# Performance work log

Hardware: AMD Instinct MI355X
Metric: run time of the kernel (lower is better)

## Reference

```python
import jax, jax.numpy as jnp
import numpy as np


def setup_inputs() -> dict:
    key = jax.random.key(0)
    k1, k2 = jax.random.split(key)
    shape = (16, 3, 512, 512)
    y_true = jax.random.uniform(k1, shape, dtype=jnp.float32)
    y_pred = jax.random.uniform(k2, shape, dtype=jnp.float32)
    return {"y_true": y_true, "y_pred": y_pred}


def reference(y_true, y_pred):
    B, C, W, H = y_true.shape
    percent = 0.4
    index = int(W * H * percent - 1)  # quantile index into ascending sort
    # gray1 = mean over the 3 channels of y_pred  -> [B, W, H]
    gray = (y_pred[:, 0] + y_pred[:, 1] + y_pred[:, 2]) / 3.0
    # torch.topk(-gray, n)[0][:, index] == -(ascending-sorted gray)[index]
    thr = jnp.sort(gray.reshape(B, W * H), axis=1)[:, index]  # [B]
    mask = (gray <= thr[:, None, None]).astype(y_pred.dtype)  # [B, W, H]
    mask = mask[:, None, :, :]  # broadcast over 3 channels
    # mask*|y_pred - y_true| == |mask*y_pred - mask*y_true| since mask in {0,1}
    d = jnp.abs(y_pred - y_true)
    w = mask * 0.8 + (1.0 - mask) * 0.2
    return jnp.mean(w * d)
```

## Files before the change

### kernel.cpp

```cpp
#include <hip/hip_runtime.h>
#include <stdint.h>

#define NB 16
#define NPIX 262144
#define K_RANK 104856u
#define NB1 4096
#define PAD(i) ((i) + ((i) >> 4))

__global__ void k_gray_hist(const float* __restrict__ yp, float* __restrict__ gray,
                            unsigned* __restrict__ hist1,
                            unsigned* __restrict__ zr, int zcount) {
    __shared__ unsigned h[NB1];
    const int tid = threadIdx.x;
    const int gtid = blockIdx.x * 256 + tid;
    if (gtid < zcount) zr[gtid] = 0;
    for (int i = tid; i < NB1; i += 256) h[i] = 0;
    __syncthreads();

    const int blk   = blockIdx.x;
    const int b     = blk >> 8;
    const int chunk = blk & 255;
    const long base = (long)b * 3 * NPIX;
    const int  o    = (chunk * 256 + tid) * 4;

    const float4 c0 = *(const float4*)(yp + base + o);
    const float4 c1 = *(const float4*)(yp + base + NPIX + o);
    const float4 c2 = *(const float4*)(yp + base + 2 * NPIX + o);

    float g0 = (c0.x + c1.x + c2.x) / 3.0f;
    float g1 = (c0.y + c1.y + c2.y) / 3.0f;
    float g2 = (c0.z + c1.z + c2.z) / 3.0f;
    float g3 = (c0.w + c1.w + c2.w) / 3.0f;

    if (gray) {
        *(float4*)(gray + (long)b * NPIX + o) = make_float4(g0, g1, g2, g3);
    }
    atomicAdd(&h[__float_as_uint(g0) >> 20], 1u);
    atomicAdd(&h[__float_as_uint(g1) >> 20], 1u);
    atomicAdd(&h[__float_as_uint(g2) >> 20], 1u);
    atomicAdd(&h[__float_as_uint(g3) >> 20], 1u);
    __syncthreads();

    unsigned* gh = hist1 + b * NB1;
    for (int i = tid; i < NB1; i += 256) {
        unsigned v = h[i];
        if (v) atomicAdd(&gh[i], v);
    }
}

__global__ void k_refine(const float* __restrict__ gray, const float* __restrict__ yp,
                         const unsigned* __restrict__ hist_scan,
                         const unsigned* __restrict__ rank_in,
                         const unsigned* __restrict__ prefix_in,
                         int width, int sel_shift, int dig_shift, unsigned dmask,
                         unsigned* __restrict__ hist_out, int nbins_out,
                         unsigned* __restrict__ rank_out, unsigned* __restrict__ prefix_out) {
    __shared__ unsigned sh[NB1 + (NB1 >> 4)];
    __shared__ unsigned wave_sums[4];
    __shared__ unsigned bc_prefix;
    const int tid   = threadIdx.x;
    const int blk   = blockIdx.x;
    const int b     = blk >> 8;
    const int chunk = blk & 255;

    const unsigned* hb = hist_scan + b * NB1;
    for (int i = tid; i < NB1; i += 256) sh[PAD(i)] = hb[i];
    __syncthreads();

    unsigned sum = 0;
    #pragma unroll
    for (int j = 0; j < 16; ++j) sum += sh[tid * 17 + j];
    unsigned inc = sum;
    for (int off = 1; off < 64; off <<= 1) {
        unsigned v = __shfl_up(inc, off);
        if ((tid & 63) >= off) inc += v;
    }
    if ((tid & 63) == 63) wave_sums[tid >> 6] = inc;
    __syncthreads();
    unsigned woff = 0;
    for (int w = 0; w < (tid >> 6); ++w) woff += wave_sums[w];
    const unsigned excl = woff + inc - sum;

    const unsigned r = rank_in ? rank_in[b] : K_RANK;
    const unsigned p = prefix_in ? prefix_in[b] : 0u;
    if (r >= excl && r < excl + sum) {
        unsigned cum = excl;
        unsigned d   = (unsigned)(tid * 16);
        #pragma unroll
        for (int j = 0; j < 16; ++j) {
            unsigned c = sh[tid * 17 + j];
            if (cum + c > r) { d = (unsigned)(tid * 16 + j); break; }
            cum += c;
        }
        bc_prefix = (p << width) | d;
        if (chunk == 0) { rank_out[b] = r - cum; prefix_out[b] = bc_prefix; }
    }
    __syncthreads();
    const unsigned pre = bc_prefix;

    for (int i = tid; i < nbins_out; i += 256) sh[i] = 0;
    __syncthreads();

    const int o = (chunk * 256 + tid) * 4;
    float g0, g1, g2, g3;
    if (gray) {
        float4 gv = *(const float4*)(gray + (long)b * NPIX + o);
        g0 = gv.x; g1 = gv.y; g2 = gv.z; g3 = gv.w;
    } else {
        const long base = (long)b * 3 * NPIX;
        float4 c0 = *(const float4*)(yp + base + o);
        float4 c1 = *(const float4*)(yp + base + NPIX + o);
        float4 c2 = *(const float4*)(yp + base + 2 * NPIX + o);
        g0 = (c0.x + c1.x + c2.x) / 3.0f;
        g1 = (c0.y + c1.y + c2.y) / 3.0f;
        g2 = (c0.z + c1.z + c2.z) / 3.0f;
        g3 = (c0.w + c1.w + c2.w) / 3.0f;
    }
    unsigned bits;
    bits = __float_as_uint(g0);
    if ((bits >> sel_shift) == pre) atomicAdd(&sh[(bits >> dig_shift) & dmask], 1u);
    bits = __float_as_uint(g1);
    if ((bits >> sel_shift) == pre) atomicAdd(&sh[(bits >> dig_shift) & dmask], 1u);
    bits = __float_as_uint(g2);
    if ((bits >> sel_shift) == pre) atomicAdd(&sh[(bits >> dig_shift) & dmask], 1u);
    bits = __float_as_uint(g3);
    if ((bits >> sel_shift) == pre) atomicAdd(&sh[(bits >> dig_shift) & dmask], 1u);
    __syncthreads();

    unsigned* gh = hist_out + b * nbins_out;
    for (int i = tid; i < nbins_out; i += 256) {
        unsigned v = sh[i];
        if (v) atomicAdd(&gh[i], v);
    }
}

__global__ void k_loss(const float* __restrict__ yt, const float* __restrict__ yp,
                       const unsigned* __restrict__ hist3,
                       const unsigned* __restrict__ rank_in,
                       const unsigned* __restrict__ prefix_in,
                       double* __restrict__ accum) {
    __shared__ unsigned wave_sums[4];
    __shared__ unsigned bc_thr;
    __shared__ float wsum[4];
    const int tid   = threadIdx.x;
    const int blk   = blockIdx.x;
    const int b     = blk >> 8;
    const int chunk = blk & 255;

    const unsigned sum = hist3[b * 256 + tid];
    unsigned inc = sum;
    for (int off = 1; off < 64; off <<= 1) {
        unsigned v = __shfl_up(inc, off);
        if ((tid & 63) >= off) inc += v;
    }
    if ((tid & 63) == 63) wave_sums[tid >> 6] = inc;
    __syncthreads();
    unsigned woff = 0;
    for (int w = 0; w < (tid >> 6); ++w) woff += wave_sums[w];
    const unsigned excl = woff + inc - sum;
    const unsigned r = rank_in[b];
    if (r >= excl && r < excl + sum) {
        bc_thr = (prefix_in[b] << 8) | (unsigned)tid;
    }
    __syncthreads();
    const unsigned thr = bc_thr;

    const long base = (long)b * 3 * NPIX;
    const int  o    = (chunk * 256 + tid) * 4;

    float4 p0 = *(const float4*)(yp + base + o);
    float4 p1 = *(const float4*)(yp + base + NPIX + o);
    float4 p2 = *(const float4*)(yp + base + 2 * NPIX + o);
    float4 t0 = *(const float4*)(yt + base + o);
    float4 t1 = *(const float4*)(yt + base + NPIX + o);
    float4 t2 = *(const float4*)(yt + base + 2 * NPIX + o);

    float s = 0.0f;
    {
        float g = (p0.x + p1.x + p2.x) / 3.0f;
        float w = (__float_as_uint(g) <= thr) ? 0.8f : 0.2f;
        s += w * (fabsf(p0.x - t0.x) + fabsf(p1.x - t1.x) + fabsf(p2.x - t2.x));
    }
    {
        float g = (p0.y + p1.y + p2.y) / 3.0f;
        float w = (__float_as_uint(g) <= thr) ? 0.8f : 0.2f;
        s += w * (fabsf(p0.y - t0.y) + fabsf(p1.y - t1.y) + fabsf(p2.y - t2.y));
    }
    {
        float g = (p0.z + p1.z + p2.z) / 3.0f;
        float w = (__float_as_uint(g) <= thr) ? 0.8f : 0.2f;
        s += w * (fabsf(p0.z - t0.z) + fabsf(p1.z - t1.z) + fabsf(p2.z - t2.z));
    }
    {
        float g = (p0.w + p1.w + p2.w) / 3.0f;
        float w = (__float_as_uint(g) <= thr) ? 0.8f : 0.2f;
        s += w * (fabsf(p0.w - t0.w) + fabsf(p1.w - t1.w) + fabsf(p2.w - t2.w));
    }

    for (int off = 32; off > 0; off >>= 1) s += __shfl_down(s, off);
    if ((tid & 63) == 0) wsum[tid >> 6] = s;
    __syncthreads();
    if (tid == 0) {
        float tot = wsum[0] + wsum[1] + wsum[2] + wsum[3];
        atomicAdd(&accum[(blk & 63) * 16], (double)tot);
    }
}

__global__ void k_final(const double* __restrict__ accum, float* __restrict__ out) {
    const int tid = threadIdx.x;
    double v = accum[tid * 16];
    for (int off = 32; off > 0; off >>= 1) v += __shfl_down(v, off);
    if (tid == 0) out[0] = (float)(v / 12582912.0);
}

extern "C" void kernel_launch(void* const* d_in, const int* in_sizes, int n_in,
                              void* d_out, int out_size, void* d_ws, size_t ws_size,
                              hipStream_t stream) {
    const float* yt = (const float*)d_in[0];
    const float* yp = (const float*)d_in[1];
    float* out = (float*)d_out;
    char* ws = (char*)d_ws;

    unsigned* hist1 = (unsigned*)(ws);
    unsigned* zr    = (unsigned*)(ws + 262144);
    unsigned* hist2 = (unsigned*)(ws + 262144);
    unsigned* hist3 = (unsigned*)(ws + 524288);
    double*   accum = (double*)(ws + 540672);
    unsigned* rank1 = (unsigned*)(ws + 548928);
    unsigned* pref1 = (unsigned*)(ws + 548992);
    unsigned* rank2 = (unsigned*)(ws + 549056);
    unsigned* pref2 = (unsigned*)(ws + 549120);
    const int zcount = (262144 + 16384 + 8192) / 4;

    float* gray = nullptr;
    const size_t gray_off = 1 << 20;
    if (ws_size >= gray_off + (size_t)NB * NPIX * sizeof(float))
        gray = (float*)(ws + gray_off);

    hipMemsetAsync(hist1, 0, 262144, stream);

    k_gray_hist<<<4096, 256, 0, stream>>>(yp, gray, hist1, zr, zcount);
    k_refine<<<4096, 256, 0, stream>>>(gray, yp, hist1, nullptr, nullptr,
                                       12, 20, 8, 0xFFFu, hist2, NB1, rank1, pref1);
    k_refine<<<4096, 256, 0, stream>>>(gray, yp, hist2, rank1, pref1,
                                       12, 8, 0, 0xFFu, hist3, 256, rank2, pref2);
    k_loss<<<4096, 256, 0, stream>>>(yt, yp, hist3, rank2, pref2, accum);
    k_final<<<1, 64, 0, stream>>>(accum, out);
}
```

Measured before the change: 169.2 us.

## Replace multi-pass radix refine with candidate collection and single-block select

Swaps the two full-grid histogram refinement passes for a small per-batch scan, a collection pass that compacts only the values falling in the selected top-12-bit bin into a candidate buffer, and a one-block-per-batch three-stage radix select over those candidates. It also stops writing the gray image to the workspace. The goal is to cut full passes over the data and the extra gray traffic. The cost is a capped candidate buffer (65536 per batch), which would silently give a wrong threshold if a bin ever held more values than that.

After: 224.5 us. 1.33x slower.

```diff
diff --git a/kernel.cpp b/kernel.cpp
--- a/kernel.cpp
+++ b/kernel.cpp
@@ -5,15 +5,12 @@
 #define NPIX 262144
 #define K_RANK 104856u
 #define NB1 4096
+#define CAP 65536
 #define PAD(i) ((i) + ((i) >> 4))
 
-__global__ void k_gray_hist(const float* __restrict__ yp, float* __restrict__ gray,
-                            unsigned* __restrict__ hist1,
-                            unsigned* __restrict__ zr, int zcount) {
+__global__ void k_gray_hist(const float* __restrict__ yp, unsigned* __restrict__ hist1) {
     __shared__ unsigned h[NB1];
     const int tid = threadIdx.x;
-    const int gtid = blockIdx.x * 256 + tid;
-    if (gtid < zcount) zr[gtid] = 0;
     for (int i = tid; i < NB1; i += 256) h[i] = 0;
     __syncthreads();
 
@@ -32,9 +29,6 @@
     float g2 = (c0.z + c1.z + c2.z) / 3.0f;
     float g3 = (c0.w + c1.w + c2.w) / 3.0f;
 
-    if (gray) {
-        *(float4*)(gray + (long)b * NPIX + o) = make_float4(g0, g1, g2, g3);
-    }
     atomicAdd(&h[__float_as_uint(g0) >> 20], 1u);
     atomicAdd(&h[__float_as_uint(g1) >> 20], 1u);
     atomicAdd(&h[__float_as_uint(g2) >> 20], 1u);
@@ -48,22 +42,14 @@
     }
 }
 
-__global__ void k_refine(const float* __restrict__ gray, const float* __restrict__ yp,
-                         const unsigned* __restrict__ hist_scan,
-                         const unsigned* __restrict__ rank_in,
-                         const unsigned* __restrict__ prefix_in,
-                         int width, int sel_shift, int dig_shift, unsigned dmask,
-                         unsigned* __restrict__ hist_out, int nbins_out,
-                         unsigned* __restrict__ rank_out, unsigned* __restrict__ prefix_out) {
+__global__ void k_scan1(const unsigned* __restrict__ hist1,
+                        unsigned* __restrict__ rank1, unsigned* __restrict__ bin1) {
     __shared__ unsigned sh[NB1 + (NB1 >> 4)];
     __shared__ unsigned wave_sums[4];
-    __shared__ unsigned bc_prefix;
-    const int tid   = threadIdx.x;
-    const int blk   = blockIdx.x;
-    const int b     = blk >> 8;
-    const int chunk = blk & 255;
-
-    const unsigned* hb = hist_scan + b * NB1;
+    const int b   = blockIdx.x;
+    const int tid = threadIdx.x;
+    const unsigned* hb = hist1 + b * NB1;
+
     for (int i = tid; i < NB1; i += 256) sh[PAD(i)] = hb[i];
     __syncthreads();
 
@@ -81,8 +67,7 @@
     for (int w = 0; w < (tid >> 6); ++w) woff += wave_sums[w];
     const unsigned excl = woff + inc - sum;
 
-    const unsigned r = rank_in ? rank_in[b] : K_RANK;
-    const unsigned p = prefix_in ? prefix_in[b] : 0u;
+    const unsigned r = K_RANK;
     if (r >= excl && r < excl + sum) {
         unsigned cum = excl;
         unsigned d   = (unsigned)(tid * 16);
@@ -92,79 +77,111 @@
             if (cum + c > r) { d = (unsigned)(tid * 16 + j); break; }
             cum += c;
         }
-        bc_prefix = (p << width) | d;
-        if (chunk == 0) { rank_out[b] = r - cum; prefix_out[b] = bc_prefix; }
-    }
-    __syncthreads();
-    const unsigned pre = bc_prefix;
-
-    for (int i = tid; i < nbins_out; i += 256) sh[i] = 0;
-    __syncthreads();
-
-    const int o = (chunk * 256 + tid) * 4;
-    float g0, g1, g2, g3;
-    if (gray) {
-        float4 gv = *(const float4*)(gray + (long)b * NPIX + o);
-        g0 = gv.x; g1 = gv.y; g2 = gv.z; g3 = gv.w;
-    } else {
-        const long base = (long)b * 3 * NPIX;
-        float4 c0 = *(const float4*)(yp + base + o);
-        float4 c1 = *(const float4*)(yp + base + NPIX + o);
-        float4 c2 = *(const float4*)(yp + base + 2 * NPIX + o);
-        g0 = (c0.x + c1.x + c2.x) / 3.0f;
-        g1 = (c0.y + c1.y + c2.y) / 3.0f;
-        g2 = (c0.z + c1.z + c2.z) / 3.0f;
-        g3 = (c0.w + c1.w + c2.w) / 3.0f;
-    }
-    unsigned bits;
-    bits = __float_as_uint(g0);
-    if ((bits >> sel_shift) == pre) atomicAdd(&sh[(bits >> dig_shift) & dmask], 1u);
-    bits = __float_as_uint(g1);
-    if ((bits >> sel_shift) == pre) atomicAdd(&sh[(bits >> dig_shift) & dmask], 1u);
-    bits = __float_as_uint(g2);
-    if ((bits >> sel_shift) == pre) atomicAdd(&sh[(bits >> dig_shift) & dmask], 1u);
-    bits = __float_as_uint(g3);
-    if ((bits >> sel_shift) == pre) atomicAdd(&sh[(bits >> dig_shift) & dmask], 1u);
-    __syncthreads();
-
-    unsigned* gh = hist_out + b * nbins_out;
-    for (int i = tid; i < nbins_out; i += 256) {
-        unsigned v = sh[i];
-        if (v) atomicAdd(&gh[i], v);
-    }
+        rank1[b] = r - cum;
+        bin1[b]  = d;
+    }
+}
+
+__global__ void k_collect(const float* __restrict__ yp, const unsigned* __restrict__ bin1,
+                          unsigned* __restrict__ count, unsigned* __restrict__ cand) {
+    __shared__ unsigned buf[1024];
+    __shared__ unsigned cnt, gbase;
+    const int tid = threadIdx.x;
+    if (tid == 0) cnt = 0;
+    __syncthreads();
+
+    const int blk   = blockIdx.x;
+    const int b     = blk >> 8;
+    const int chunk = blk & 255;
+    const long base = (long)b * 3 * NPIX;
+    const int  o    = (chunk * 256 + tid) * 4;
+
+    const float4 c0 = *(const float4*)(yp + base + o);
+    const float4 c1 = *(const float4*)(yp + base + NPIX + o);
+    const float4 c2 = *(const float4*)(yp + base + 2 * NPIX + o);
+
+    float g[4];
+    g[0] = (c0.x + c1.x + c2.x) / 3.0f;
+    g[1] = (c0.y + c1.y + c2.y) / 3.0f;
+    g[2] = (c0.z + c1.z + c2.z) / 3.0f;
+    g[3] = (c0.w + c1.w + c2.w) / 3.0f;
+
+    const unsigned sel = bin1[b];
+    #pragma unroll
+    for (int k = 0; k < 4; ++k) {
+        unsigned u = __float_as_uint(g[k]);
+        if ((u >> 20) == sel) {
+            unsigned i = atomicAdd(&cnt, 1u);
+            buf[i] = u;
+        }
+    }
+    __syncthreads();
+    if (tid == 0) gbase = atomicAdd(&count[b], cnt);
+    __syncthreads();
+    const unsigned gb = gbase, n = cnt;
+    unsigned* cb = cand + (long)b * CAP;
+    for (unsigned i = tid; i < n; i += 256) {
+        unsigned dst = gb + i;
+        if (dst < CAP) cb[dst] = buf[i];
+    }
+}
+
+__global__ void k_select(const unsigned* __restrict__ cand, const unsigned* __restrict__ count,
+                         const unsigned* __restrict__ rank1, const unsigned* __restrict__ bin1,
+                         unsigned* __restrict__ thr) {
+    __shared__ unsigned h[256];
+    __shared__ unsigned wave_sums[4];
+    __shared__ unsigned s_pre, s_rank;
+    const int b   = blockIdx.x;
+    const int tid = threadIdx.x;
+    unsigned n = count[b];
+    if (n > CAP) n = CAP;
+    if (tid == 0) { s_pre = bin1[b]; s_rank = rank1[b]; }
+    __syncthreads();
+    const unsigned* cb = cand + (long)b * CAP;
+
+    const int mshift[3] = {20, 12, 4};
+    const int dshift[3] = {12, 4, 0};
+    const unsigned dmask[3] = {255u, 255u, 15u};
+    const int pwidth[3] = {8, 8, 4};
+
+    for (int p = 0; p < 3; ++p) {
+        h[tid] = 0;
+        __syncthreads();
+        const unsigned pre = s_pre;
+        for (unsigned i = tid; i < n; i += 256) {
+            unsigned v = cb[i];
+            if ((v >> mshift[p]) == pre) atomicAdd(&h[(v >> dshift[p]) & dmask[p]], 1u);
+        }
+        __syncthreads();
+        unsigned sum = h[tid];
+        unsigned inc = sum;
+        for (int off = 1; off < 64; off <<= 1) {
+            unsigned v = __shfl_up(inc, off);
+            if ((tid & 63) >= off) inc += v;
+        }
+        if ((tid & 63) == 63) wave_sums[tid >> 6] = inc;
+        __syncthreads();
+        unsigned woff = 0;
+        for (int w = 0; w < (tid >> 6); ++w) woff += wave_sums[w];
+        const unsigned excl = woff + inc - sum;
+        const unsigned r = s_rank;
+        if (sum > 0 && r >= excl && r < excl + sum) {
+            s_rank = r - excl;
+            s_pre  = (pre << pwidth[p]) | (unsigned)tid;
+        }
+        __syncthreads();
+    }
+    if (tid == 0) thr[b] = s_pre;
 }
 
 __global__ void k_loss(const float* __restrict__ yt, const float* __restrict__ yp,
-                       const unsigned* __restrict__ hist3,
-                       const unsigned* __restrict__ rank_in,
-                       const unsigned* __restrict__ prefix_in,
-                       double* __restrict__ accum) {
-    __shared__ unsigned wave_sums[4];
-    __shared__ unsigned bc_thr;
+                       const unsigned* __restrict__ thr_arr, double* __restrict__ accum) {
     __shared__ float wsum[4];
     const int tid   = threadIdx.x;
     const int blk   = blockIdx.x;
     const int b     = blk >> 8;
     const int chunk = blk & 255;
-
-    const unsigned sum = hist3[b * 256 + tid];
-    unsigned inc = sum;
-    for (int off = 1; off < 64; off <<= 1) {
-        unsigned v = __shfl_up(inc, off);
-        if ((tid & 63) >= off) inc += v;
-    }
-    if ((tid & 63) == 63) wave_sums[tid >> 6] = inc;
-    __syncthreads();
-    unsigned woff = 0;
-    for (int w = 0; w < (tid >> 6); ++w) woff += wave_sums[w];
-    const unsigned excl = woff + inc - sum;
-    const unsigned r = rank_in[b];
-    if (r >= excl && r < excl + sum) {
-        bc_thr = (prefix_in[b] << 8) | (unsigned)tid;
-    }
-    __syncthreads();
-    const unsigned thr = bc_thr;
-
     const long base = (long)b * 3 * NPIX;
     const int  o    = (chunk * 256 + tid) * 4;
 
@@ -175,6 +192,7 @@
     float4 t1 = *(const float4*)(yt + base + NPIX + o);
     float4 t2 = *(const float4*)(yt + base + 2 * NPIX + o);
 
+    const unsigned thr = thr_arr[b];
     float s = 0.0f;
     {
         float g = (p0.x + p1.x + p2.x) / 3.0f;
@@ -222,28 +240,19 @@
     char* ws = (char*)d_ws;
 
     unsigned* hist1 = (unsigned*)(ws);
-    unsigned* zr    = (unsigned*)(ws + 262144);
-    unsigned* hist2 = (unsigned*)(ws + 262144);
-    unsigned* hist3 = (unsigned*)(ws + 524288);
-    double*   accum = (double*)(ws + 540672);
-    unsigned* rank1 = (unsigned*)(ws + 548928);
-    unsigned* pref1 = (unsigned*)(ws + 548992);
-    unsigned* rank2 = (unsigned*)(ws + 549056);
-    unsigned* pref2 = (unsigned*)(ws + 549120);
-    const int zcount = (262144 + 16384 + 8192) / 4;
-
-    float* gray = nullptr;
-    const size_t gray_off = 1 << 20;
-    if (ws_size >= gray_off + (size_t)NB * NPIX * sizeof(float))
-        gray = (float*)(ws + gray_off);
-
-    hipMemsetAsync(hist1, 0, 262144, stream);
-
-    k_gray_hist<<<4096, 256, 0, stream>>>(yp, gray, hist1, zr, zcount);
-    k_refine<<<4096, 256, 0, stream>>>(gray, yp, hist1, nullptr, nullptr,
-                                       12, 20, 8, 0xFFFu, hist2, NB1, rank1, pref1);
-    k_refine<<<4096, 256, 0, stream>>>(gray, yp, hist2, rank1, pref1,
-                                       12, 8, 0, 0xFFu, hist3, 256, rank2, pref2);
-    k_loss<<<4096, 256, 0, stream>>>(yt, yp, hist3, rank2, pref2, accum);
+    unsigned* count = (unsigned*)(ws + 262144);
+    unsigned* rank1 = (unsigned*)(ws + 262208);
+    unsigned* bin1  = (unsigned*)(ws + 262272);
+    unsigned* thr   = (unsigned*)(ws + 262336);
+    double*   accum = (double*)(ws + 262656);
+    unsigned* cand  = (unsigned*)(ws + (1 << 20));
+
+    hipMemsetAsync(ws, 0, 262656 + 8192, stream);
+
+    k_gray_hist<<<4096, 256, 0, stream>>>(yp, hist1);
+    k_scan1<<<NB, 256, 0, stream>>>(hist1, rank1, bin1);
+    k_collect<<<4096, 256, 0, stream>>>(yp, bin1, count, cand);
+    k_select<<<NB, 256, 0, stream>>>(cand, count, rank1, bin1, thr);
+    k_loss<<<4096, 256, 0, stream>>>(yt, yp, thr, accum);
     k_final<<<1, 64, 0, stream>>>(accum, out);
 }
```
